# Kernel tuning notes

Measured on AMD Instinct MI355X. Metric: run time of the kernel, lower is better.

The kernel has to match this reference:

```python
import jax, jax.numpy as jnp
import numpy as np

T = 8          # message-passing steps (hparams['T'])
D = 64         # link_state_dim
R = 128        # readout_units
E = 100000     # num edges (rows of link_state)
M = 400000     # num messages (len of states_first/second)
G = 1000       # num graphs in the batch


def _gru_cell(x, h, W, U, b):
    """Keras GRUCell with reset_after=True. x:[N,in], h:[N,units].
    W:[in,3u], U:[u,3u], b:[2,3u] (input bias, recurrent bias)."""
    mx = x @ W + b[0]
    mh = h @ U + b[1]
    xz, xr, xh = jnp.split(mx, 3, axis=-1)
    hz, hr, hh = jnp.split(mh, 3, axis=-1)
    z = jax.nn.sigmoid(xz + hz)
    r = jax.nn.sigmoid(xr + hr)
    cand = jnp.tanh(xh + r * hh)
    return z * h + (1.0 - z) * cand


def setup_inputs() -> dict:
    key = jax.random.key(0)
    ks = jax.random.split(key, 12)
    glorot = jax.nn.initializers.glorot_uniform()
    inp = {
        "link_state": jax.random.normal(ks[0], (E, D), jnp.float32),
        "states_first": jax.random.randint(ks[1], (M,), 0, E, jnp.int32),
        "states_second": jax.random.randint(ks[2], (M,), 0, E, jnp.int32),
        "states_graph_ids": jnp.sort(jax.random.randint(ks[3], (E,), 0, G, jnp.int32)),
        "num_edges": E,
        # Message MLP: Dense(D) with selu on concat [*, 2D]
        "W_msg": glorot(ks[4], (2 * D, D), jnp.float32),
        "b_msg": jnp.zeros((D,), jnp.float32),
        # Update GRUCell (units=D, input dim=D)
        "W_upd": glorot(ks[5], (D, 3 * D), jnp.float32),
        "U_upd": glorot(ks[6], (D, 3 * D), jnp.float32),
        "b_upd": jnp.zeros((2, 3 * D), jnp.float32),
        # Readout GRU (units=R, input dim=D)
        "W_ro": glorot(ks[7], (D, 3 * R), jnp.float32),
        "U_ro": glorot(ks[8], (R, 3 * R), jnp.float32),
        "b_ro": jnp.zeros((2, 3 * R), jnp.float32),
        # Final Dense(1)
        "W_out": glorot(ks[9], (R, 1), jnp.float32),
        "b_out": jnp.zeros((1,), jnp.float32),
    }
    return inp


def reference(link_state, states_first, states_second, states_graph_ids, num_edges,
              W_msg, b_msg, W_upd, U_upd, b_upd, W_ro, U_ro, b_ro, W_out, b_out):
    def mp_step(h, _):
        # gather sender/receiver states, concat -> message MLP (selu)
        edges_concat = jnp.concatenate([h[states_first], h[states_second]], axis=1)  # [M, 2D]
        msg = jax.nn.selu(edges_concat @ W_msg + b_msg)                              # [M, D]
        # scatter-add messages to receiver edges
        agg = jax.ops.segment_sum(msg, states_second, num_segments=num_edges)        # [E, D]
        h_new = _gru_cell(agg, h, W_upd, U_upd, b_upd)                               # [E, D]
        return h_new, h_new

    _, seq = jax.lax.scan(mp_step, link_state, None, length=T)  # seq: [T, E, D]

    # Readout GRU over the T-step state sequence per edge; return last hidden state
    def ro_step(h, x_t):
        h_new = _gru_cell(x_t, h, W_ro, U_ro, b_ro)
        return h_new, None

    h0 = jnp.zeros((link_state.shape[0], R), link_state.dtype)
    historial, _ = jax.lax.scan(ro_step, h0, seq)               # [E, R]

    # sorted segment_sum over graph ids, then Dense(1)
    per_graph = jax.ops.segment_sum(historial, states_graph_ids, num_segments=G,
                                    indices_are_sorted=True)    # [G, R]
    return per_graph @ W_out + b_out                             # [G, 1]
```

## Files before the change

kernel.cpp:

```cpp
#include <hip/hip_runtime.h>
#include <hip/hip_bf16.h>

#define D 64
#define R 128
#define NSTEPS 8
#define SELU_SCALE 1.0507009873554805f
#define SELU_ALPHA 1.6732632423543772f
#define PADH 72
#define PADF 68
#define PADR 136

typedef _Float16 half8 __attribute__((ext_vector_type(8)));
typedef float f32x4 __attribute__((ext_vector_type(4)));

__device__ __forceinline__ float fast_sig(float x) {
    return __fdividef(1.0f, 1.0f + __expf(-x));
}
__device__ __forceinline__ float fast_tanh(float x) {
    float xc = fminf(fmaxf(x, -15.0f), 15.0f);
    float e = __expf(2.0f * xc);
    return 1.0f - __fdividef(2.0f, e + 1.0f);
}

__global__ __launch_bounds__(256) void swizzle_all(
    const float* __restrict__ Wm, const float* __restrict__ Wu,
    const float* __restrict__ Uu, const float* __restrict__ Wr,
    const float* __restrict__ Ur,
    _Float16* __restrict__ wWm, _Float16* __restrict__ wWu,
    _Float16* __restrict__ wUu, _Float16* __restrict__ wWr,
    _Float16* __restrict__ wUr)
{
    const float* src; _Float16* dst; int K, N;
    switch (blockIdx.y) {
        case 0: src = Wm; dst = wWm; K = 128; N = 64;  break;
        case 1: src = Wu; dst = wWu; K = 64;  N = 192; break;
        case 2: src = Uu; dst = wUu; K = 64;  N = 192; break;
        case 3: src = Wr; dst = wWr; K = 64;  N = 384; break;
        default: src = Ur; dst = wUr; K = 128; N = 384; break;
    }
    int idx = blockIdx.x * 256 + threadIdx.x;
    int KT = K >> 5;
    int total = KT * (N >> 4) * 512;
    if (idx >= total) return;
    int j = idx & 7;
    int lane = (idx >> 3) & 63;
    int kt = (idx >> 9) % KT;
    int nt = idx / (512 * KT);
    int k = 32 * kt + 8 * (lane >> 4) + j;
    int n = 16 * nt + (lane & 15);
    dst[idx] = (_Float16)src[(size_t)k * N + n];
}

__global__ __launch_bounds__(256) void h16_init(const float* __restrict__ src,
                                                _Float16* __restrict__ dst, int n) {
    int i = blockIdx.x * 256 + threadIdx.x;
    if (i < n) dst[i] = (_Float16)src[i];
}

__global__ __launch_bounds__(192) void bias_pack(const float* __restrict__ bu,
                                                 const float* __restrict__ brr,
                                                 float4* __restrict__ biasU,
                                                 float4* __restrict__ biasR) {
    int c = threadIdx.x;
    if (c < 64) {
        biasU[c] = make_float4(bu[c] + bu[192 + c], bu[64 + c] + bu[256 + c],
                               bu[128 + c], bu[320 + c]);
    } else {
        int cr = c - 64;
        biasR[cr] = make_float4(brr[cr] + brr[384 + cr], brr[128 + cr] + brr[512 + cr],
                                brr[256 + cr], brr[640 + cr]);
    }
}

__global__ __launch_bounds__(256) void hist_kernel(const int* __restrict__ second,
                                                   int* __restrict__ cnt, int M) {
    int m = blockIdx.x * 256 + threadIdx.x;
    if (m < M) atomicAdd(&cnt[second[m]], 1);
}

__global__ __launch_bounds__(256) void scan_bsum(const int* __restrict__ cnt,
                                                 int* __restrict__ bsum, int E) {
    int i = blockIdx.x * 256 + threadIdx.x;
    int tid = threadIdx.x;
    int v = (i < E) ? cnt[i] : 0;
    __shared__ int s[256];
    s[tid] = v;
    __syncthreads();
    #pragma unroll
    for (int d = 1; d < 256; d <<= 1) {
        int t = (tid >= d) ? s[tid - d] : 0;
        __syncthreads();
        s[tid] += t;
        __syncthreads();
    }
    if (tid == 255) bsum[blockIdx.x] = s[255];
}

__global__ __launch_bounds__(1024) void scan_part(int* __restrict__ bsum, int NB) {
    int tid = threadIdx.x;
    __shared__ int s[1024];
    int v = (tid < NB) ? bsum[tid] : 0;
    s[tid] = v;
    __syncthreads();
    #pragma unroll
    for (int d = 1; d < 1024; d <<= 1) {
        int t = (tid >= d) ? s[tid - d] : 0;
        __syncthreads();
        s[tid] += t;
        __syncthreads();
    }
    if (tid < NB) bsum[tid] = s[tid] - v;
}

__global__ __launch_bounds__(256) void scan_final(const int* __restrict__ cnt,
                                                  const int* __restrict__ bsum,
                                                  int* __restrict__ off, int E) {
    int i = blockIdx.x * 256 + threadIdx.x;
    int tid = threadIdx.x;
    int v = (i < E) ? cnt[i] : 0;
    __shared__ int s[256];
    s[tid] = v;
    __syncthreads();
    #pragma unroll
    for (int d = 1; d < 256; d <<= 1) {
        int t = (tid >= d) ? s[tid - d] : 0;
        __syncthreads();
        s[tid] += t;
        __syncthreads();
    }
    if (i < E) off[i] = bsum[blockIdx.x] + s[tid] - v;
}

__global__ __launch_bounds__(256) void scatter_kernel(const int* __restrict__ second,
                                                      const int* __restrict__ off,
                                                      int* __restrict__ cur,
                                                      int* __restrict__ perm, int M) {
    int m = blockIdx.x * 256 + threadIdx.x;
    if (m < M) {
        int s = second[m];
        int p = atomicAdd(&cur[s], 1);
        perm[off[s] + p] = m;
    }
}

__global__ __launch_bounds__(256) void bucket_sort(const int* __restrict__ off,
                                                   int* __restrict__ perm,
                                                   int E, int M) {
    int e = blockIdx.x * 256 + threadIdx.x;
    if (e >= E) return;
    int a = off[e];
    int b = (e == E - 1) ? M : off[e + 1];
    for (int i = a + 1; i < b; ++i) {
        int key = perm[i];
        int j = i - 1;
        while (j >= a && perm[j] > key) {
            perm[j + 1] = perm[j];
            --j;
        }
        perm[j + 1] = key;
    }
}

__global__ __launch_bounds__(256) void fs_pack(const int* __restrict__ first,
                                               const int* __restrict__ second,
                                               const int* __restrict__ perm,
                                               int2* __restrict__ fs, int M) {
    int m = blockIdx.x * 256 + threadIdx.x;
    if (m < M) {
        int pm = perm[m];
        fs[m] = make_int2(first[pm], second[pm]);
    }
}

__global__ __launch_bounds__(256) void msg_upd(
    const _Float16* __restrict__ hin,
    _Float16* __restrict__ hout,
    const int2* __restrict__ fs,
    const int* __restrict__ off,
    const half8* __restrict__ wBm,
    const float* __restrict__ bm,
    const half8* __restrict__ wWu,
    const half8* __restrict__ wUu,
    const float4* __restrict__ biasU,
    int E, int M)
{
    __shared__ _Float16 stage_s[4][16 * PADH];
    __shared__ float aggF_s[4][16 * PADF];
    __shared__ int skeys[4][16];

    const int wid = threadIdx.x >> 6;
    const int lane = threadIdx.x & 63;
    const int hi = lane >> 4;
    const int l15 = lane & 15;
    const int e0 = (blockIdx.x * 4 + wid) * 16;

    _Float16* stageH = stage_s[wid];
    float* aggF = aggF_s[wid];
    int* skey = skeys[wid];

    #pragma unroll
    for (int m = 0; m < 16; ++m)
        aggF[m * PADF + lane] = 0.0f;

    half8 Bm[4][4];
    #pragma unroll
    for (int nt = 0; nt < 4; ++nt)
        #pragma unroll
        for (int kt = 0; kt < 4; ++kt)
            Bm[nt][kt] = wBm[(nt * 4 + kt) * 64 + lane];

    if (e0 >= E) return;

    {
        int b = min(e0 + 16, E);
        int mstart = off[e0];
        int mend = (b == E) ? M : off[b];

        #pragma unroll 1
        for (int ch = 0; mstart + ch * 16 < mend; ++ch) {
            int mrow = mstart + ch * 16 + l15;
            bool mv = (mrow < mend);
            int mcl = min(mrow, mend - 1);
            int2 p = fs[mcl];
            const half8* fr = reinterpret_cast<const half8*>(hin + (size_t)p.x * D);
            const half8* sr = reinterpret_cast<const half8*>(hin + (size_t)p.y * D);
            half8 A[4];
            A[0] = fr[hi];
            A[1] = fr[4 + hi];
            A[2] = sr[hi];
            A[3] = sr[4 + hi];

            f32x4 acc[4];
            #pragma unroll
            for (int nt = 0; nt < 4; ++nt) acc[nt] = (f32x4){0.f, 0.f, 0.f, 0.f};
            #pragma unroll
            for (int nt = 0; nt < 4; ++nt)
                #pragma unroll
                for (int kt = 0; kt < 4; ++kt)
                    acc[nt] = __builtin_amdgcn_mfma_f32_16x16x32_f16(A[kt], Bm[nt][kt], acc[nt], 0, 0, 0);

            #pragma unroll
            for (int nt = 0; nt < 4; ++nt) {
                int n = nt * 16 + l15;
                float bias = bm[n];
                #pragma unroll
                for (int r = 0; r < 4; ++r) {
                    float v = acc[nt][r] + bias;
                    v = (v > 0.0f) ? (SELU_SCALE * v)
                                   : (SELU_SCALE * SELU_ALPHA) * (__expf(v) - 1.0f);
                    stageH[(hi * 4 + r) * PADH + n] = (_Float16)v;
                }
            }
            if (lane < 16) skey[lane] = mv ? (p.y - e0) : -1;

            float run = 0.0f;
            int kprev = skey[0];
            #pragma unroll
            for (int m = 0; m < 16; ++m) {
                int km = skey[m];
                if (km != kprev) {
                    if (kprev >= 0) aggF[kprev * PADF + lane] += run;
                    run = 0.0f;
                    kprev = km;
                }
                run += (float)stageH[m * PADH + lane];
            }
            if (kprev >= 0) aggF[kprev * PADF + lane] += run;
        }
    }

    const int ec = min(e0 + l15, E - 1);

    half8 AX[2], AHu[2];
    #pragma unroll
    for (int kt = 0; kt < 2; ++kt) {
        const float* s = aggF + l15 * PADF + 32 * kt + 8 * hi;
        half8 ax;
        #pragma unroll
        for (int j = 0; j < 8; ++j) ax[j] = (_Float16)s[j];
        AX[kt] = ax;
        AHu[kt] = reinterpret_cast<const half8*>(hin + (size_t)ec * D)[4 * kt + hi];
    }

    #pragma unroll 1
    for (int i = 0; i < 4; ++i) {
        half8 WBz[2], WBr[2], WBc[2], UBz[2], UBr[2], UBc[2];
        #pragma unroll
        for (int kt = 0; kt < 2; ++kt) {
            WBz[kt] = wWu[((0 + i) * 2 + kt) * 64 + lane];
            WBr[kt] = wWu[((4 + i) * 2 + kt) * 64 + lane];
            WBc[kt] = wWu[((8 + i) * 2 + kt) * 64 + lane];
            UBz[kt] = wUu[((0 + i) * 2 + kt) * 64 + lane];
            UBr[kt] = wUu[((4 + i) * 2 + kt) * 64 + lane];
            UBc[kt] = wUu[((8 + i) * 2 + kt) * 64 + lane];
        }
        int n = 16 * i + l15;
        float4 bU = biasU[n];

        f32x4 az  = (f32x4){0.f, 0.f, 0.f, 0.f};
        f32x4 ar_ = (f32x4){0.f, 0.f, 0.f, 0.f};
        f32x4 acx = (f32x4){0.f, 0.f, 0.f, 0.f};
        f32x4 ach = (f32x4){0.f, 0.f, 0.f, 0.f};
        #pragma unroll
        for (int kt = 0; kt < 2; ++kt) {
            az  = __builtin_amdgcn_mfma_f32_16x16x32_f16(AX[kt], WBz[kt], az, 0, 0, 0);
            az  = __builtin_amdgcn_mfma_f32_16x16x32_f16(AHu[kt], UBz[kt], az, 0, 0, 0);
            ar_ = __builtin_amdgcn_mfma_f32_16x16x32_f16(AX[kt], WBr[kt], ar_, 0, 0, 0);
            ar_ = __builtin_amdgcn_mfma_f32_16x16x32_f16(AHu[kt], UBr[kt], ar_, 0, 0, 0);
            acx = __builtin_amdgcn_mfma_f32_16x16x32_f16(AX[kt], WBc[kt], acx, 0, 0, 0);
            ach = __builtin_amdgcn_mfma_f32_16x16x32_f16(AHu[kt], UBc[kt], ach, 0, 0, 0);
        }
        #pragma unroll
        for (int r = 0; r < 4; ++r) {
            int e = e0 + hi * 4 + r;
            int ecl = min(e, E - 1);
            float z = fast_sig(az[r] + bU.x);
            float rr = fast_sig(ar_[r] + bU.y);
            float c = fast_tanh(acx[r] + bU.z + rr * (ach[r] + bU.w));
            float hp = (float)hin[(size_t)ecl * D + n];
            float hn = z * hp + (1.0f - z) * c;
            if (e < E) hout[(size_t)e * D + n] = (_Float16)hn;
        }
    }
}

__global__ __launch_bounds__(512, 2) void ro_all(
    const _Float16* __restrict__ hseq1,
    const int* __restrict__ gid,
    const float* __restrict__ Wout,
    const half8* __restrict__ wWr,
    const half8* __restrict__ wUr,
    const float4* __restrict__ biasR,
    float* __restrict__ out,
    int E, int edelems)
{
    __shared__ _Float16 rotile[16 * PADR];
    __shared__ float partials[8][16];

    const int w = threadIdx.x >> 6;
    const int lane = threadIdx.x & 63;
    const int hi = lane >> 4;
    const int l15 = lane & 15;
    const int e0 = blockIdx.x * 16;
    const int ec = min(e0 + l15, E - 1);

    half8 WBz[2], WBr[2], WBx[2], UBz[4], UBr[4], UBh[4];
    #pragma unroll
    for (int kt = 0; kt < 2; ++kt) {
        WBz[kt] = wWr[((0 + w) * 2 + kt) * 64 + lane];
        WBr[kt] = wWr[((8 + w) * 2 + kt) * 64 + lane];
        WBx[kt] = wWr[((16 + w) * 2 + kt) * 64 + lane];
    }
    #pragma unroll
    for (int kt = 0; kt < 4; ++kt) {
        UBz[kt] = wUr[((0 + w) * 4 + kt) * 64 + lane];
        UBr[kt] = wUr[((8 + w) * 4 + kt) * 64 + lane];
        UBh[kt] = wUr[((16 + w) * 4 + kt) * 64 + lane];
    }
    const int c = w * 16 + l15;
    const float4 bR = biasR[c];

    half8 hp = {};

    #pragma unroll 1
    for (int t = 0; t < NSTEPS; ++t) {
        #pragma unroll
        for (int r = 0; r < 4; ++r)
            rotile[(hi * 4 + r) * PADR + w * 16 + l15] = hp[r];
        __syncthreads();

        half8 AHro[4];
        #pragma unroll
        for (int kt = 0; kt < 4; ++kt)
            AHro[kt] = *reinterpret_cast<const half8*>(&rotile[l15 * PADR + 32 * kt + 8 * hi]);
        __syncthreads();

        const _Float16* ht = hseq1 + (size_t)t * edelems;
        half8 AXt[2];
        #pragma unroll
        for (int kt = 0; kt < 2; ++kt)
            AXt[kt] = reinterpret_cast<const half8*>(ht + (size_t)ec * D)[4 * kt + hi];

        f32x4 az  = (f32x4){0.f, 0.f, 0.f, 0.f};
        f32x4 ar_ = (f32x4){0.f, 0.f, 0.f, 0.f};
        f32x4 acx = (f32x4){0.f, 0.f, 0.f, 0.f};
        f32x4 ach = (f32x4){0.f, 0.f, 0.f, 0.f};
        #pragma unroll
        for (int kt = 0; kt < 2; ++kt) {
            az  = __builtin_amdgcn_mfma_f32_16x16x32_f16(AXt[kt], WBz[kt], az, 0, 0, 0);
            ar_ = __builtin_amdgcn_mfma_f32_16x16x32_f16(AXt[kt], WBr[kt], ar_, 0, 0, 0);
            acx = __builtin_amdgcn_mfma_f32_16x16x32_f16(AXt[kt], WBx[kt], acx, 0, 0, 0);
        }
        #pragma unroll
        for (int kt = 0; kt < 4; ++kt) {
            az  = __builtin_amdgcn_mfma_f32_16x16x32_f16(AHro[kt], UBz[kt], az, 0, 0, 0);
            ar_ = __builtin_amdgcn_mfma_f32_16x16x32_f16(AHro[kt], UBr[kt], ar_, 0, 0, 0);
            ach = __builtin_amdgcn_mfma_f32_16x16x32_f16(AHro[kt], UBh[kt], ach, 0, 0, 0);
        }
        #pragma unroll
        for (int r = 0; r < 4; ++r) {
            float z = fast_sig(az[r] + bR.x);
            float rr = fast_sig(ar_[r] + bR.y);
            float cc = fast_tanh(acx[r] + bR.z + rr * (ach[r] + bR.w));
            float hpf = (float)hp[r];
            hp[r] = (_Float16)(z * hpf + (1.0f - z) * cc);
        }
    }

    const float wv = Wout[c];
    float part[4];
    #pragma unroll
    for (int r = 0; r < 4; ++r) part[r] = (float)hp[r] * wv;
    #pragma unroll
    for (int d = 1; d < 16; d <<= 1) {
        #pragma unroll
        for (int r = 0; r < 4; ++r)
            part[r] += __shfl_xor(part[r], d);
    }
    if (l15 == 0) {
        #pragma unroll
        for (int r = 0; r < 4; ++r)
            partials[w][hi * 4 + r] = part[r];
    }
    __syncthreads();
    if (w == 0 && lane < 16) {
        float s = 0.0f;
        #pragma unroll
        for (int ww = 0; ww < 8; ++ww) s += partials[ww][lane];
        int e = e0 + lane;
        if (e < E) unsafeAtomicAdd(out + gid[e], s);
    }
}

__global__ void out_init_kernel(float* __restrict__ out, const float* __restrict__ b_out, int G) {
    int g = blockIdx.x * blockDim.x + threadIdx.x;
    if (g < G) out[g] = b_out[0];
}

extern "C" void kernel_launch(void* const* d_in, const int* in_sizes, int n_in,
                              void* d_out, int out_size, void* d_ws, size_t ws_size,
                              hipStream_t stream) {
    const float* link_state = (const float*)d_in[0];
    const int*   first      = (const int*)d_in[1];
    const int*   second     = (const int*)d_in[2];
    const int*   gids       = (const int*)d_in[3];
    const float* Wm         = (const float*)d_in[5];
    const float* bm         = (const float*)d_in[6];
    const float* Wu         = (const float*)d_in[7];
    const float* Uu         = (const float*)d_in[8];
    const float* bu         = (const float*)d_in[9];
    const float* Wr         = (const float*)d_in[10];
    const float* Ur         = (const float*)d_in[11];
    const float* brb        = (const float*)d_in[12];
    const float* Wout       = (const float*)d_in[13];
    const float* bout       = (const float*)d_in[14];

    const int E = in_sizes[0] / D;
    const int M = in_sizes[1];
    const int G = out_size;

    char* p = (char*)d_ws;
    auto carve = [&](size_t bytes) {
        void* r = (void*)p;
        p += (bytes + 255) & ~(size_t)255;
        return r;
    };
    const size_t edelems = (size_t)E * D;
    _Float16*  hseq  = (_Float16*)carve(edelems * 2 * (NSTEPS + 1));
    int*       perm  = (int*)carve((size_t)M * 4);
    int2*      fs    = (int2*)carve((size_t)M * 8);
    int*       cnt   = (int*)carve((size_t)E * 4);
    int*       cur   = (int*)carve((size_t)E * 4);
    int*       off   = (int*)carve((size_t)(E + 1) * 4);
    int*       bsum  = (int*)carve(4096 * 4);
    _Float16*  wWm   = (_Float16*)carve(8192 * 2);
    _Float16*  wWu   = (_Float16*)carve(12288 * 2);
    _Float16*  wUu   = (_Float16*)carve(12288 * 2);
    _Float16*  wWr   = (_Float16*)carve(24576 * 2);
    _Float16*  wUr   = (_Float16*)carve(49152 * 2);
    float4*    biasU = (float4*)carve(64 * 16);
    float4*    biasR = (float4*)carve(128 * 16);

    hipMemsetAsync(cnt, 0, (size_t)E * 4, stream);
    hipMemsetAsync(cur, 0, (size_t)E * 4, stream);

    h16_init<<<(E * D + 255) / 256, 256, 0, stream>>>(link_state, hseq, E * D);
    swizzle_all<<<dim3(192, 5), 256, 0, stream>>>(Wm, Wu, Uu, Wr, Ur,
                                                  wWm, wWu, wUu, wWr, wUr);
    bias_pack<<<1, 192, 0, stream>>>(bu, brb, biasU, biasR);

    const int NB = (E + 255) / 256;
    hist_kernel<<<(M + 255) / 256, 256, 0, stream>>>(second, cnt, M);
    scan_bsum<<<NB, 256, 0, stream>>>(cnt, bsum, E);
    scan_part<<<1, 1024, 0, stream>>>(bsum, NB);
    scan_final<<<NB, 256, 0, stream>>>(cnt, bsum, off, E);
    scatter_kernel<<<(M + 255) / 256, 256, 0, stream>>>(second, off, cur, perm, M);
    bucket_sort<<<NB, 256, 0, stream>>>(off, perm, E, M);
    fs_pack<<<(M + 255) / 256, 256, 0, stream>>>(first, second, perm, fs, M);

    const int e_blocks = (E + 63) / 64;

    for (int t = 0; t < NSTEPS; ++t) {
        msg_upd<<<e_blocks, 256, 0, stream>>>(hseq + (size_t)t * edelems,
                                              hseq + (size_t)(t + 1) * edelems,
                                              fs, off,
                                              (const half8*)wWm, bm,
                                              (const half8*)wWu, (const half8*)wUu, biasU,
                                              E, M);
    }

    out_init_kernel<<<(G + 255) / 256, 256, 0, stream>>>((float*)d_out, bout, G);
    const int ro_blocks = (E + 15) / 16;
    ro_all<<<ro_blocks, 512, 0, stream>>>(hseq + edelems, gids, Wout,
                                          (const half8*)wWr, (const half8*)wUr, biasR,
                                          (float*)d_out, E, (int)edelems);
}
```

Baseline: 806.0 us.

## Process two 16-edge tiles per readout block to amortize weight loads and syncs

The readout GRU kernel now handles 32 edges per block as two independent 16-row tiles that share the register-resident weight fragments. Per step, the input loads for both tiles are issued before the LDS exchange, the two sync barriers now cover twice the work, and the MFMA chains of the two tiles are interleaved for more instruction-level parallelism. The launch-bounds minimum-occupancy hint is dropped, so register pressure rises and occupancy may fall. The block count is halved.

```diff
diff --git a/kernel.cpp b/kernel.cpp
--- a/kernel.cpp
+++ b/kernel.cpp
@@ -324,7 +324,7 @@
     }
 }
 
-__global__ __launch_bounds__(512, 2) void ro_all(
+__global__ __launch_bounds__(512) void ro_all(
     const _Float16* __restrict__ hseq1,
     const int* __restrict__ gid,
     const float* __restrict__ Wout,
@@ -334,15 +334,17 @@
     float* __restrict__ out,
     int E, int edelems)
 {
-    __shared__ _Float16 rotile[16 * PADR];
-    __shared__ float partials[8][16];
+    __shared__ _Float16 rotA[16 * PADR];
+    __shared__ _Float16 rotB[16 * PADR];
+    __shared__ float partials[8][32];
 
     const int w = threadIdx.x >> 6;
     const int lane = threadIdx.x & 63;
     const int hi = lane >> 4;
     const int l15 = lane & 15;
-    const int e0 = blockIdx.x * 16;
-    const int ec = min(e0 + l15, E - 1);
+    const int e0 = blockIdx.x * 32;
+    const int ecA = min(e0 + l15, E - 1);
+    const int ecB = min(e0 + 16 + l15, E - 1);
 
     half8 WBz[2], WBr[2], WBx[2], UBz[4], UBr[4], UBh[4];
     #pragma unroll
@@ -360,70 +362,105 @@
     const int c = w * 16 + l15;
     const float4 bR = biasR[c];
 
-    half8 hp = {};
+    half8 hpA = {}, hpB = {};
 
     #pragma unroll 1
     for (int t = 0; t < NSTEPS; ++t) {
-        #pragma unroll
-        for (int r = 0; r < 4; ++r)
-            rotile[(hi * 4 + r) * PADR + w * 16 + l15] = hp[r];
-        __syncthreads();
-
-        half8 AHro[4];
-        #pragma unroll
-        for (int kt = 0; kt < 4; ++kt)
-            AHro[kt] = *reinterpret_cast<const half8*>(&rotile[l15 * PADR + 32 * kt + 8 * hi]);
-        __syncthreads();
-
         const _Float16* ht = hseq1 + (size_t)t * edelems;
-        half8 AXt[2];
-        #pragma unroll
-        for (int kt = 0; kt < 2; ++kt)
-            AXt[kt] = reinterpret_cast<const half8*>(ht + (size_t)ec * D)[4 * kt + hi];
-
-        f32x4 az  = (f32x4){0.f, 0.f, 0.f, 0.f};
-        f32x4 ar_ = (f32x4){0.f, 0.f, 0.f, 0.f};
-        f32x4 acx = (f32x4){0.f, 0.f, 0.f, 0.f};
-        f32x4 ach = (f32x4){0.f, 0.f, 0.f, 0.f};
+        half8 AXtA[2], AXtB[2];
         #pragma unroll
         for (int kt = 0; kt < 2; ++kt) {
-            az  = __builtin_amdgcn_mfma_f32_16x16x32_f16(AXt[kt], WBz[kt], az, 0, 0, 0);
-            ar_ = __builtin_amdgcn_mfma_f32_16x16x32_f16(AXt[kt], WBr[kt], ar_, 0, 0, 0);
-            acx = __builtin_amdgcn_mfma_f32_16x16x32_f16(AXt[kt], WBx[kt], acx, 0, 0, 0);
-        }
-        #pragma unroll
-        for (int kt = 0; kt < 4; ++kt) {
-            az  = __builtin_amdgcn_mfma_f32_16x16x32_f16(AHro[kt], UBz[kt], az, 0, 0, 0);
-            ar_ = __builtin_amdgcn_mfma_f32_16x16x32_f16(AHro[kt], UBr[kt], ar_, 0, 0, 0);
-            ach = __builtin_amdgcn_mfma_f32_16x16x32_f16(AHro[kt], UBh[kt], ach, 0, 0, 0);
-        }
+            AXtA[kt] = reinterpret_cast<const half8*>(ht + (size_t)ecA * D)[4 * kt + hi];
+            AXtB[kt] = reinterpret_cast<const half8*>(ht + (size_t)ecB * D)[4 * kt + hi];
+        }
+
         #pragma unroll
         for (int r = 0; r < 4; ++r) {
-            float z = fast_sig(az[r] + bR.x);
-            float rr = fast_sig(ar_[r] + bR.y);
-            float cc = fast_tanh(acx[r] + bR.z + rr * (ach[r] + bR.w));
-            float hpf = (float)hp[r];
-            hp[r] = (_Float16)(z * hpf + (1.0f - z) * cc);
+            rotA[(hi * 4 + r) * PADR + w * 16 + l15] = hpA[r];
+            rotB[(hi * 4 + r) * PADR + w * 16 + l15] = hpB[r];
+        }
+        __syncthreads();
+
+        f32x4 azA = (f32x4){0.f,0.f,0.f,0.f}, arA = (f32x4){0.f,0.f,0.f,0.f};
+        f32x4 axA = (f32x4){0.f,0.f,0.f,0.f}, ahA = (f32x4){0.f,0.f,0.f,0.f};
+        f32x4 azB = (f32x4){0.f,0.f,0.f,0.f}, arB = (f32x4){0.f,0.f,0.f,0.f};
+        f32x4 axB = (f32x4){0.f,0.f,0.f,0.f}, ahB = (f32x4){0.f,0.f,0.f,0.f};
+        #pragma unroll
+        for (int kt = 0; kt < 2; ++kt) {
+            azA = __builtin_amdgcn_mfma_f32_16x16x32_f16(AXtA[kt], WBz[kt], azA, 0, 0, 0);
+            azB = __builtin_amdgcn_mfma_f32_16x16x32_f16(AXtB[kt], WBz[kt], azB, 0, 0, 0);
+            arA = __builtin_amdgcn_mfma_f32_16x16x32_f16(AXtA[kt], WBr[kt], arA, 0, 0, 0);
+            arB = __builtin_amdgcn_mfma_f32_16x16x32_f16(AXtB[kt], WBr[kt], arB, 0, 0, 0);
+            axA = __builtin_amdgcn_mfma_f32_16x16x32_f16(AXtA[kt], WBx[kt], axA, 0, 0, 0);
+            axB = __builtin_amdgcn_mfma_f32_16x16x32_f16(AXtB[kt], WBx[kt], axB, 0, 0, 0);
+        }
+
+        {
+            half8 AHro[4];
+            #pragma unroll
+            for (int kt = 0; kt < 4; ++kt)
+                AHro[kt] = *reinterpret_cast<const half8*>(&rotA[l15 * PADR + 32 * kt + 8 * hi]);
+            #pragma unroll
+            for (int kt = 0; kt < 4; ++kt) {
+                azA = __builtin_amdgcn_mfma_f32_16x16x32_f16(AHro[kt], UBz[kt], azA, 0, 0, 0);
+                arA = __builtin_amdgcn_mfma_f32_16x16x32_f16(AHro[kt], UBr[kt], arA, 0, 0, 0);
+                ahA = __builtin_amdgcn_mfma_f32_16x16x32_f16(AHro[kt], UBh[kt], ahA, 0, 0, 0);
+            }
+        }
+        {
+            half8 AHro[4];
+            #pragma unroll
+            for (int kt = 0; kt < 4; ++kt)
+                AHro[kt] = *reinterpret_cast<const half8*>(&rotB[l15 * PADR + 32 * kt + 8 * hi]);
+            #pragma unroll
+            for (int kt = 0; kt < 4; ++kt) {
+                azB = __builtin_amdgcn_mfma_f32_16x16x32_f16(AHro[kt], UBz[kt], azB, 0, 0, 0);
+                arB = __builtin_amdgcn_mfma_f32_16x16x32_f16(AHro[kt], UBr[kt], arB, 0, 0, 0);
+                ahB = __builtin_amdgcn_mfma_f32_16x16x32_f16(AHro[kt], UBh[kt], ahB, 0, 0, 0);
+            }
+        }
+        __syncthreads();
+
+        #pragma unroll
+        for (int r = 0; r < 4; ++r) {
+            float zA = fast_sig(azA[r] + bR.x);
+            float rrA = fast_sig(arA[r] + bR.y);
+            float ccA = fast_tanh(axA[r] + bR.z + rrA * (ahA[r] + bR.w));
+            float hA = (float)hpA[r];
+            hpA[r] = (_Float16)(zA * hA + (1.0f - zA) * ccA);
+
+            float zB = fast_sig(azB[r] + bR.x);
+            float rrB = fast_sig(arB[r] + bR.y);
+            float ccB = fast_tanh(axB[r] + bR.z + rrB * (ahB[r] + bR.w));
+            float hB = (float)hpB[r];
+            hpB[r] = (_Float16)(zB * hB + (1.0f - zB) * ccB);
         }
     }
 
     const float wv = Wout[c];
-    float part[4];
-    #pragma unroll
-    for (int r = 0; r < 4; ++r) part[r] = (float)hp[r] * wv;
+    float pA[4], pB[4];
+    #pragma unroll
+    for (int r = 0; r < 4; ++r) {
+        pA[r] = (float)hpA[r] * wv;
+        pB[r] = (float)hpB[r] * wv;
+    }
     #pragma unroll
     for (int d = 1; d < 16; d <<= 1) {
         #pragma unroll
-        for (int r = 0; r < 4; ++r)
-            part[r] += __shfl_xor(part[r], d);
+        for (int r = 0; r < 4; ++r) {
+            pA[r] += __shfl_xor(pA[r], d);
+            pB[r] += __shfl_xor(pB[r], d);
+        }
     }
     if (l15 == 0) {
         #pragma unroll
-        for (int r = 0; r < 4; ++r)
-            partials[w][hi * 4 + r] = part[r];
+        for (int r = 0; r < 4; ++r) {
+            partials[w][hi * 4 + r] = pA[r];
+            partials[w][16 + hi * 4 + r] = pB[r];
+        }
     }
     __syncthreads();
-    if (w == 0 && lane < 16) {
+    if (w == 0 && lane < 32) {
         float s = 0.0f;
         #pragma unroll
         for (int ww = 0; ww < 8; ++ww) s += partials[ww][lane];
@@ -510,7 +547,7 @@
     }
 
     out_init_kernel<<<(G + 255) / 256, 256, 0, stream>>>((float*)d_out, bout, G);
-    const int ro_blocks = (E + 15) / 16;
+    const int ro_blocks = (E + 31) / 32;
     ro_all<<<ro_blocks, 512, 0, stream>>>(hseq + edelems, gids, Wout,
                                           (const half8*)wWr, (const half8*)wUr, biasR,
                                           (float*)d_out, E, (int)edelems);
```

Result: slower. 843.8 us (+4.7%).
